# Kernel tuning notes

Hardware: AMD Instinct MI355X
Metric: run time of the kernel (lower is better)

Reference implementation:

```python
import jax, jax.numpy as jnp
import numpy as np

D_MODEL = 1024
NHEAD = 16
D_K = D_MODEL // NHEAD


def setup_inputs() -> dict:
    key = jax.random.key(0)
    ks = jax.random.split(key, 12)
    B, L = 4, 2048
    s = 1.0 / np.sqrt(D_MODEL)
    inp = {
        "query": jax.random.normal(ks[0], (B, L, D_MODEL), jnp.float32),
        "key": jax.random.normal(ks[1], (B, L, D_MODEL), jnp.float32),
        "value": jax.random.normal(ks[2], (B, L, D_MODEL), jnp.float32),
        "Wq": jax.random.normal(ks[3], (D_MODEL, D_MODEL), jnp.float32) * s,
        "bq": jnp.zeros((D_MODEL,), jnp.float32),
        "Wk": jax.random.normal(ks[4], (D_MODEL, D_MODEL), jnp.float32) * s,
        "bk": jnp.zeros((D_MODEL,), jnp.float32),
        "Wv": jax.random.normal(ks[5], (D_MODEL, D_MODEL), jnp.float32) * s,
        "bv": jnp.zeros((D_MODEL,), jnp.float32),
        "Wo": jax.random.normal(ks[6], (D_MODEL, D_MODEL), jnp.float32) * s,
        "bo": jnp.zeros((D_MODEL,), jnp.float32),
    }
    return inp


def reference(query, key, value, Wq, bq, Wk, bk, Wv, bv, Wo, bo):
    B, Lq, _ = query.shape
    Lk = key.shape[1]
    # Linear projections, split into heads: [B, H, L, d_k]
    Q = (query @ Wq + bq).reshape(B, Lq, NHEAD, D_K).transpose(0, 2, 1, 3)
    K = (key @ Wk + bk).reshape(B, Lk, NHEAD, D_K).transpose(0, 2, 1, 3)
    V = (value @ Wv + bv).reshape(B, Lk, NHEAD, D_K).transpose(0, 2, 1, 3)
    scale = 1.0 / jnp.sqrt(jnp.asarray(D_K, Q.dtype))
    scores = jnp.einsum("bhqd,bhkd->bhqk", Q, K) * scale  # [B,H,Lq,Lk]
    attn = jax.nn.softmax(scores, axis=-1)
    context = jnp.einsum("bhqk,bhkd->bhqd", attn, V)
    context = context.transpose(0, 2, 1, 3).reshape(B, Lq, D_MODEL)
    return context @ Wo + bo
```

## Files before the change

kernel.cpp:

```cpp
#include <hip/hip_runtime.h>
#include <hip/hip_bf16.h>
#include <cstdint>
#include <cstddef>


typedef unsigned short u16;
typedef __bf16 bf8v __attribute__((ext_vector_type(8)));
typedef __bf16 bf4v __attribute__((ext_vector_type(4)));
typedef float f32x4 __attribute__((ext_vector_type(4)));

#define D_MODEL 1024
#define NHEAD   16
#define DK      64
#define BATCH   4
#define SEQ     2048
#define ROWS    (BATCH * SEQ)

__device__ __forceinline__ u16 f2b(float f) {
  union { float f; unsigned int i; } x; x.f = f;
  unsigned int r = x.i + 0x7fffu + ((x.i >> 16) & 1u);
  return (u16)(r >> 16);
}
__device__ __forceinline__ ushort4 pack4(float a, float b, float c, float d) {
  union { bf4v v; ushort4 u; } x;
  x.v[0] = (__bf16)a; x.v[1] = (__bf16)b; x.v[2] = (__bf16)c; x.v[3] = (__bf16)d;
  return x.u;
}
__device__ __forceinline__ bf8v cvt8(float4 a, float4 b) {
  bf8v r;
  r[0] = (__bf16)a.x; r[1] = (__bf16)a.y; r[2] = (__bf16)a.z; r[3] = (__bf16)a.w;
  r[4] = (__bf16)b.x; r[5] = (__bf16)b.y; r[6] = (__bf16)b.z; r[7] = (__bf16)b.w;
  return r;
}
__device__ __forceinline__ void async16(const void* g, void* l) {
  __builtin_amdgcn_global_load_lds((const __attribute__((address_space(1))) void*)g,
                                   (__attribute__((address_space(3))) void*)l, 16, 0, 0);
}
#define MFMA16(a, b, c) __builtin_amdgcn_mfma_f32_16x16x32_bf16(a, b, c, 0, 0, 0)

__global__ void wtrans_cvt_kernel(const float* __restrict__ w0, const float* __restrict__ w1,
                                  const float* __restrict__ w2, const float* __restrict__ w3,
                                  u16* __restrict__ dst4) {
  __shared__ float t[32][33];
  const float* src = (blockIdx.z == 0) ? w0 : (blockIdx.z == 1) ? w1
                   : (blockIdx.z == 2) ? w2 : w3;
  u16* dst = dst4 + (size_t)blockIdx.z * D_MODEL * D_MODEL;
  const int c0 = blockIdx.x * 32, r0 = blockIdx.y * 32;
  for (int i = threadIdx.y; i < 32; i += 8)
    t[i][threadIdx.x] = src[(size_t)(r0 + i) * D_MODEL + c0 + threadIdx.x];
  __syncthreads();
  for (int i = threadIdx.y; i < 32; i += 8)
    dst[(size_t)(c0 + i) * D_MODEL + r0 + threadIdx.x] = f2b(t[threadIdx.x][i]);
}

#define BM 128
#define BN 128
#define BK 32

__global__ __launch_bounds__(256, 2) void gemm_qkv(
    const float* __restrict__ Aq, const float* __restrict__ Ak,
    const float* __restrict__ Av, const u16* __restrict__ wt,
    const float* __restrict__ bq, const float* __restrict__ bk,
    const float* __restrict__ bv, u16* __restrict__ Qw, u16* __restrict__ Kw,
    u16* __restrict__ Vt, float qscale) {
  __shared__ __align__(16) u16 As[2][BM * BK];
  __shared__ __align__(16) u16 Bs[2][BN * BK];
  const int z = blockIdx.y;
  const float* A = (z == 0) ? Aq : (z == 1) ? Ak : Av;
  const u16* Bt = wt + (size_t)z * D_MODEL * D_MODEL;
  const float* bias = (z == 0) ? bq : (z == 1) ? bk : bv;
  u16* out = (z == 0) ? Qw : (z == 1) ? Kw : Vt;
  const float oscale = (z == 0) ? qscale : 1.0f;

  const int lid = blockIdx.x;
  const int xcd = lid & 7, jj = lid >> 3;
  const int m0 = ((xcd << 3) + (jj >> 3)) * BM;
  const int n0 = (jj & 7) * BN;

  const int tid = threadIdx.x;
  const int lane = tid & 63, wave = tid >> 6;
  const int wm = wave >> 1, wn = wave & 1;
  const int quad = lane >> 4, l16 = lane & 15;
  const int K = 1024;

  f32x4 acc[4][4];
#pragma unroll
  for (int i = 0; i < 4; i++)
#pragma unroll
    for (int j = 0; j < 4; j++) acc[i][j] = (f32x4){0.f, 0.f, 0.f, 0.f};

  const int srow = tid >> 2;
  const int sch = ((tid & 3) ^ ((tid >> 3) & 3)) * 8;
  const int fsw = (quad ^ ((l16 >> 1) & 3)) * 8;
  const float* Ag0 = A + (size_t)(m0 + srow) * K + sch;
  const float* Ag1 = Ag0 + (size_t)64 * K;
  const u16* Bg = Bt + (size_t)(n0 + srow) * K + sch;

  float4 a0 = *(const float4*)(Ag0);
  float4 a1 = *(const float4*)(Ag0 + 4);
  float4 a2 = *(const float4*)(Ag1);
  float4 a3 = *(const float4*)(Ag1 + 4);
  async16(Bg, &Bs[0][tid * 8]);
  async16(Bg + (size_t)64 * K, &Bs[0][2048 + tid * 8]);
  *(bf8v*)&As[0][tid * 8]        = cvt8(a0, a1);
  *(bf8v*)&As[0][2048 + tid * 8] = cvt8(a2, a3);
  a0 = *(const float4*)(Ag0 + BK);
  a1 = *(const float4*)(Ag0 + BK + 4);
  a2 = *(const float4*)(Ag1 + BK);
  a3 = *(const float4*)(Ag1 + BK + 4);
  __syncthreads();

  int p = 0;
  for (int k0 = 0; k0 < K; k0 += BK) {
    const int kn = k0 + BK;
    if (kn < K) {
      async16(Bg + kn, &Bs[p ^ 1][tid * 8]);
      async16(Bg + (size_t)64 * K + kn, &Bs[p ^ 1][2048 + tid * 8]);
      *(bf8v*)&As[p ^ 1][tid * 8]        = cvt8(a0, a1);
      *(bf8v*)&As[p ^ 1][2048 + tid * 8] = cvt8(a2, a3);
      if (kn + BK < K) {
        a0 = *(const float4*)(Ag0 + kn + BK);
        a1 = *(const float4*)(Ag0 + kn + BK + 4);
        a2 = *(const float4*)(Ag1 + kn + BK);
        a3 = *(const float4*)(Ag1 + kn + BK + 4);
      }
    }

    bf8v af[4], bfr[4];
#pragma unroll
    for (int i = 0; i < 4; i++)
      af[i] = *(const bf8v*)&As[p][(wm * 64 + i * 16 + l16) * BK + fsw];
#pragma unroll
    for (int j = 0; j < 4; j++)
      bfr[j] = *(const bf8v*)&Bs[p][(wn * 64 + j * 16 + l16) * BK + fsw];
    if (z < 2) {
#pragma unroll
      for (int i = 0; i < 4; i++)
#pragma unroll
        for (int j = 0; j < 4; j++)
          acc[i][j] = MFMA16(bfr[j], af[i], acc[i][j]);
    } else {
#pragma unroll
      for (int i = 0; i < 4; i++)
#pragma unroll
        for (int j = 0; j < 4; j++)
          acc[i][j] = MFMA16(af[i], bfr[j], acc[i][j]);
    }
    __syncthreads();
    p ^= 1;
  }

  if (z < 2) {
#pragma unroll
    for (int i = 0; i < 4; i++) {
      const int m = m0 + wm * 64 + i * 16 + l16;
      const int b = m >> 11, l = m & 2047;
#pragma unroll
      for (int j = 0; j < 4; j++) {
        const int n = n0 + wn * 64 + j * 16 + quad * 4;
        const float4 bv4 = *(const float4*)&bias[n];
        const int h = n >> 6, d = n & 63;
        *(ushort4*)&out[(((size_t)(b * NHEAD + h) * SEQ + l) << 6) + d] =
            pack4((acc[i][j][0] + bv4.x) * oscale, (acc[i][j][1] + bv4.y) * oscale,
                  (acc[i][j][2] + bv4.z) * oscale, (acc[i][j][3] + bv4.w) * oscale);
      }
    }
  } else {
#pragma unroll
    for (int j = 0; j < 4; j++) {
      const int n = n0 + wn * 64 + j * 16 + l16;
      const float bvs = bias[n];
      const int h = n >> 6, d = n & 63;
#pragma unroll
      for (int i = 0; i < 4; i++) {
        const int row = m0 + wm * 64 + i * 16 + quad * 4;
        const int b = row >> 11, l = row & 2047;
        const int pl = (l & ~31) | ((l & 12) << 1) | ((l & 16) >> 2);
        *(ushort4*)&out[(((size_t)(b * NHEAD + h) * DK + d) << 11) + pl] =
            pack4(acc[i][j][0] + bvs, acc[i][j][1] + bvs,
                  acc[i][j][2] + bvs, acc[i][j][3] + bvs);
      }
    }
  }
}

__global__ __launch_bounds__(256, 2) void gemm_out(const u16* __restrict__ A,
                                                   const u16* __restrict__ Bt,
                                                   const float* __restrict__ bias,
                                                   float* __restrict__ out) {
  __shared__ __align__(16) u16 As[2][BM * BK];
  __shared__ __align__(16) u16 Bs[2][BN * BK];
  const int lid = blockIdx.x;
  const int xcd = lid & 7, jj = lid >> 3;
  const int m0 = ((xcd << 3) + (jj >> 3)) * BM;
  const int n0 = (jj & 7) * BN;
  const int tid = threadIdx.x;
  const int lane = tid & 63, wave = tid >> 6;
  const int wm = wave >> 1, wn = wave & 1;
  const int quad = lane >> 4, l16 = lane & 15;
  const int K = 1024;

  f32x4 acc[4][4];
#pragma unroll
  for (int i = 0; i < 4; i++)
#pragma unroll
    for (int j = 0; j < 4; j++) acc[i][j] = (f32x4){0.f, 0.f, 0.f, 0.f};

  const int srow = tid >> 2;
  const int sch = ((tid & 3) ^ ((tid >> 3) & 3)) * 8;
  const int fsw = (quad ^ ((l16 >> 1) & 3)) * 8;
  const u16* Ag = A + (size_t)(m0 + srow) * K + sch;
  const u16* Bg = Bt + (size_t)(n0 + srow) * K + sch;

  async16(Ag, &As[0][tid * 8]);
  async16(Ag + (size_t)64 * K, &As[0][2048 + tid * 8]);
  async16(Bg, &Bs[0][tid * 8]);
  async16(Bg + (size_t)64 * K, &Bs[0][2048 + tid * 8]);
  __syncthreads();

  int p = 0;
  for (int k0 = 0; k0 < K; k0 += BK) {
    const int kn = k0 + BK;
    if (kn < K) {
      async16(Ag + kn, &As[p ^ 1][tid * 8]);
      async16(Ag + (size_t)64 * K + kn, &As[p ^ 1][2048 + tid * 8]);
      async16(Bg + kn, &Bs[p ^ 1][tid * 8]);
      async16(Bg + (size_t)64 * K + kn, &Bs[p ^ 1][2048 + tid * 8]);
    }

    bf8v af[4], bfr[4];
#pragma unroll
    for (int i = 0; i < 4; i++)
      af[i] = *(const bf8v*)&As[p][(wm * 64 + i * 16 + l16) * BK + fsw];
#pragma unroll
    for (int j = 0; j < 4; j++)
      bfr[j] = *(const bf8v*)&Bs[p][(wn * 64 + j * 16 + l16) * BK + fsw];
#pragma unroll
    for (int i = 0; i < 4; i++)
#pragma unroll
      for (int j = 0; j < 4; j++)
        acc[i][j] = MFMA16(bfr[j], af[i], acc[i][j]);
    __syncthreads();
    p ^= 1;
  }

#pragma unroll
  for (int i = 0; i < 4; i++) {
    const int m = m0 + wm * 64 + i * 16 + l16;
#pragma unroll
    for (int j = 0; j < 4; j++) {
      const int n = n0 + wn * 64 + j * 16 + quad * 4;
      const float4 bv4 = *(const float4*)&bias[n];
      float4 vv;
      vv.x = acc[i][j][0] + bv4.x; vv.y = acc[i][j][1] + bv4.y;
      vv.z = acc[i][j][2] + bv4.z; vv.w = acc[i][j][3] + bv4.w;
      *(float4*)&out[(size_t)m * D_MODEL + n] = vv;
    }
  }
}

__global__ __launch_bounds__(256, 4) void attn_kernel(const u16* __restrict__ Q,
                                                      const u16* __restrict__ K,
                                                      const u16* __restrict__ Vt,
                                                      u16* __restrict__ ctx) {
  const int bh = blockIdx.x;
  const int qb = blockIdx.y * 128;
  const int tid = threadIdx.x;
  const int lane = tid & 63, wave = tid >> 6;
  const int quad = lane >> 4, l16 = lane & 15;
  const u16* Qh = Q + (size_t)bh * SEQ * DK;
  const u16* Kh = K + (size_t)bh * SEQ * DK;
  const u16* Vh = Vt + (size_t)bh * DK * SEQ;

  __shared__ __align__(16) u16 Ks[2][2][64 * 32];
  __shared__ __align__(16) u16 Vs[2][64 * 64];

  const int srow = tid >> 2;
  const int sch  = ((tid & 3) ^ ((tid >> 3) & 3)) * 8;
  const int ldst = tid * 8;
  const int fsw  = (quad ^ ((l16 >> 1) & 3)) * 8;
  const int vd   = tid >> 3;
  const int vcol = ((tid & 7) ^ ((tid >> 3) & 7)) * 8;

  bf8v qf[2][2];
#pragma unroll
  for (int qg = 0; qg < 2; qg++)
#pragma unroll
    for (int h = 0; h < 2; h++)
      qf[qg][h] = *(const bf8v*)&Qh[(size_t)(qb + wave * 32 + qg * 16 + l16) * DK + h * 32 + quad * 8];

  bf8v ones;
#pragma unroll
  for (int j = 0; j < 8; j++) ones[j] = (__bf16)1.0f;

  f32x4 o[2][4];
  f32x4 la[2];
  float m_q[2];
#pragma unroll
  for (int qg = 0; qg < 2; qg++) {
    m_q[qg] = -1e30f; la[qg] = (f32x4){0.f, 0.f, 0.f, 0.f};
#pragma unroll
    for (int d = 0; d < 4; d++) o[qg][d] = (f32x4){0.f, 0.f, 0.f, 0.f};
  }

  async16(Kh + (size_t)srow * DK + sch,      &Ks[0][0][ldst]);
  async16(Kh + (size_t)srow * DK + 32 + sch, &Ks[0][1][ldst]);
  async16(Vh + (size_t)vd * SEQ + vcol,        &Vs[0][ldst]);
  async16(Vh + (size_t)(vd + 32) * SEQ + vcol, &Vs[0][2048 + ldst]);
  __syncthreads();

  int p = 0;
  for (int kt = 0; kt < SEQ; kt += 64) {
    const int nt = kt + 64;
    if (nt < SEQ) {
      async16(Kh + (size_t)(nt + srow) * DK + sch,      &Ks[p ^ 1][0][ldst]);
      async16(Kh + (size_t)(nt + srow) * DK + 32 + sch, &Ks[p ^ 1][1][ldst]);
      async16(Vh + (size_t)vd * SEQ + nt + vcol,        &Vs[p ^ 1][ldst]);
      async16(Vh + (size_t)(vd + 32) * SEQ + nt + vcol, &Vs[p ^ 1][2048 + ldst]);
    }

    bf8v kf[4][2];
#pragma unroll
    for (int nb = 0; nb < 4; nb++)
#pragma unroll
      for (int h = 0; h < 2; h++)
        kf[nb][h] = *(const bf8v*)&Ks[p][h][(nb * 16 + l16) * 32 + fsw];

    bf8v pf[2][2];
#pragma unroll
    for (int qg = 0; qg < 2; qg++) {
      f32x4 s[4];
      __builtin_amdgcn_s_setprio(1);
#pragma unroll
      for (int nb = 0; nb < 4; nb++) {
        f32x4 t = (f32x4){0.f, 0.f, 0.f, 0.f};
        t = MFMA16(kf[nb][0], qf[qg][0], t);
        t = MFMA16(kf[nb][1], qf[qg][1], t);
        s[nb] = t;
      }
      __builtin_amdgcn_s_setprio(0);
      float t0 = fmaxf(fmaxf(s[0][0], s[0][1]), fmaxf(s[0][2], s[0][3]));
      float t1 = fmaxf(fmaxf(s[1][0], s[1][1]), fmaxf(s[1][2], s[1][3]));
      float t2 = fmaxf(fmaxf(s[2][0], s[2][1]), fmaxf(s[2][2], s[2][3]));
      float t3 = fmaxf(fmaxf(s[3][0], s[3][1]), fmaxf(s[3][2], s[3][3]));
      float mx = fmaxf(fmaxf(t0, t1), fmaxf(t2, t3));
      mx = fmaxf(mx, __shfl_xor(mx, 16));
      mx = fmaxf(mx, __shfl_xor(mx, 32));
      const float mprev = m_q[qg];
      float Mn = mprev;
      const int resc = !__all(mx - mprev <= 8.0f);
      if (resc) {
        Mn = fmaxf(mprev, mx);
        const float al = __builtin_amdgcn_exp2f(mprev - Mn);
        m_q[qg] = Mn;
        la[qg] *= al;
#pragma unroll
        for (int d = 0; d < 4; d++) o[qg][d] *= al;
      }
#pragma unroll
      for (int nb = 0; nb < 4; nb++)
#pragma unroll
        for (int r = 0; r < 4; r++)
          s[nb][r] = __builtin_amdgcn_exp2f(s[nb][r] - Mn);
#pragma unroll
      for (int kc = 0; kc < 2; kc++) {
        bf8v pw;
#pragma unroll
        for (int j = 0; j < 4; j++) {
          pw[j]     = (__bf16)s[2 * kc][j];
          pw[j + 4] = (__bf16)s[2 * kc + 1][j];
        }
        pf[qg][kc] = pw;
      }
      la[qg] = MFMA16(ones, pf[qg][0], la[qg]);
      la[qg] = MFMA16(ones, pf[qg][1], la[qg]);
    }

    bf8v vf[4][2];
#pragma unroll
    for (int dc = 0; dc < 4; dc++) {
      const int rb = (dc * 16 + l16) * 64;
#pragma unroll
      for (int kc = 0; kc < 2; kc++)
        vf[dc][kc] = *(const bf8v*)&Vs[p][rb + (((kc * 4 + quad) ^ (l16 & 7)) * 8)];
    }
    __builtin_amdgcn_s_setprio(1);
#pragma unroll
    for (int qg = 0; qg < 2; qg++)
#pragma unroll
      for (int dc = 0; dc < 4; dc++) {
        o[qg][dc] = MFMA16(vf[dc][0], pf[qg][0], o[qg][dc]);
        o[qg][dc] = MFMA16(vf[dc][1], pf[qg][1], o[qg][dc]);
      }
    __builtin_amdgcn_s_setprio(0);

    __syncthreads();
    p ^= 1;
  }

  const int b = bh >> 4, hh = bh & 15;
#pragma unroll
  for (int qg = 0; qg < 2; qg++) {
    const float inv = __builtin_amdgcn_rcpf(la[qg][0]);
    const int q = qb + wave * 32 + qg * 16 + l16;
#pragma unroll
    for (int dc = 0; dc < 4; dc++) {
      const int col = hh * 64 + dc * 16 + quad * 4;
      *(ushort4*)&ctx[(size_t)(b * SEQ + q) * D_MODEL + col] =
          pack4(o[qg][dc][0] * inv, o[qg][dc][1] * inv,
                o[qg][dc][2] * inv, o[qg][dc][3] * inv);
    }
  }
}

extern "C" void kernel_launch(void* const* d_in, const int* in_sizes, int n_in,
                              void* d_out, int out_size, void* d_ws, size_t ws_size,
                              hipStream_t stream) {
  const float* q  = (const float*)d_in[0];
  const float* k  = (const float*)d_in[1];
  const float* v  = (const float*)d_in[2];
  const float* Wq = (const float*)d_in[3];
  const float* bq = (const float*)d_in[4];
  const float* Wk = (const float*)d_in[5];
  const float* bk = (const float*)d_in[6];
  const float* Wv = (const float*)d_in[7];
  const float* bv = (const float*)d_in[8];
  const float* Wo = (const float*)d_in[9];
  const float* bo = (const float*)d_in[10];

  u16* ws  = (u16*)d_ws;
  u16* wt  = ws;
  u16* Qw  = wt + (size_t)4 * D_MODEL * D_MODEL;
  u16* Kw  = Qw + (size_t)ROWS * D_MODEL;
  u16* Vt  = Kw + (size_t)ROWS * D_MODEL;
  u16* ctx = Vt + (size_t)ROWS * D_MODEL;

  const float QSCALE = 0.18033688011112042f;

  wtrans_cvt_kernel<<<dim3(32, 32, 4), dim3(32, 8), 0, stream>>>(Wq, Wk, Wv, Wo, wt);

  gemm_qkv<<<dim3(512, 3), 256, 0, stream>>>(q, k, v, wt, bq, bk, bv, Qw, Kw, Vt, QSCALE);

  attn_kernel<<<dim3(BATCH * NHEAD, SEQ / 128), 256, 0, stream>>>(Qw, Kw, Vt, ctx);

  gemm_out<<<512, 256, 0, stream>>>(ctx, wt + (size_t)3 * D_MODEL * D_MODEL, bo,
                                    (float*)d_out);
}
```

Baseline: 384.0 us.

## Double GEMM K-tile depth to 64 with wider swizzle and MFMA priority

Raises BK from 32 to 64 in the QKV and output-projection GEMMs, which halves the number of K iterations and barriers. The load mapping and the XOR swizzle are reworked for 64-wide rows (8 chunks per row, 4 row groups per thread). The change also brackets the MFMA block with s_setprio so that compute waves get priority. Shared memory doubles to 64KB per block, which may limit occupancy at the 2-block launch bound, and register pressure grows from the extra prefetch registers.

```diff
diff --git a/kernel.cpp b/kernel.cpp
--- a/kernel.cpp
+++ b/kernel.cpp
@@ -55,7 +55,8 @@
 
 #define BM 128
 #define BN 128
-#define BK 32
+#define BK 64
+#define NT (1024 / BK)
 
 __global__ __launch_bounds__(256, 2) void gemm_qkv(
     const float* __restrict__ Aq, const float* __restrict__ Ak,
@@ -89,63 +90,82 @@
 #pragma unroll
     for (int j = 0; j < 4; j++) acc[i][j] = (f32x4){0.f, 0.f, 0.f, 0.f};
 
-  const int srow = tid >> 2;
-  const int sch = ((tid & 3) ^ ((tid >> 3) & 3)) * 8;
-  const int fsw = (quad ^ ((l16 >> 1) & 3)) * 8;
-  const float* Ag0 = A + (size_t)(m0 + srow) * K + sch;
-  const float* Ag1 = Ag0 + (size_t)64 * K;
-  const u16* Bg = Bt + (size_t)(n0 + srow) * K + sch;
-
-  float4 a0 = *(const float4*)(Ag0);
-  float4 a1 = *(const float4*)(Ag0 + 4);
-  float4 a2 = *(const float4*)(Ag1);
-  float4 a3 = *(const float4*)(Ag1 + 4);
-  async16(Bg, &Bs[0][tid * 8]);
-  async16(Bg + (size_t)64 * K, &Bs[0][2048 + tid * 8]);
-  *(bf8v*)&As[0][tid * 8]        = cvt8(a0, a1);
-  *(bf8v*)&As[0][2048 + tid * 8] = cvt8(a2, a3);
-  a0 = *(const float4*)(Ag0 + BK);
-  a1 = *(const float4*)(Ag0 + BK + 4);
-  a2 = *(const float4*)(Ag1 + BK);
-  a3 = *(const float4*)(Ag1 + BK + 4);
+  const int s8 = tid >> 3;
+  const int lc = ((tid & 7) ^ ((tid >> 4) & 7)) * 8;
+  const int fk = (l16 >> 1) & 7;
+  const float* Agt = A + (size_t)(m0 + s8) * K + lc;
+  const u16* Bgt = Bt + (size_t)(n0 + s8) * K + lc;
+
+  float4 ar[8];
+#pragma unroll
+  for (int m = 0; m < 4; m++) {
+    ar[2 * m]     = *(const float4*)(Agt + (size_t)m * 32 * K);
+    ar[2 * m + 1] = *(const float4*)(Agt + (size_t)m * 32 * K + 4);
+  }
+#pragma unroll
+  for (int m = 0; m < 4; m++)
+    async16(Bgt + (size_t)m * 32 * K, &Bs[0][m * 2048 + tid * 8]);
+#pragma unroll
+  for (int m = 0; m < 4; m++)
+    *(bf8v*)&As[0][m * 2048 + tid * 8] = cvt8(ar[2 * m], ar[2 * m + 1]);
+#pragma unroll
+  for (int m = 0; m < 4; m++) {
+    ar[2 * m]     = *(const float4*)(Agt + (size_t)m * 32 * K + BK);
+    ar[2 * m + 1] = *(const float4*)(Agt + (size_t)m * 32 * K + BK + 4);
+  }
   __syncthreads();
 
   int p = 0;
-  for (int k0 = 0; k0 < K; k0 += BK) {
-    const int kn = k0 + BK;
+  for (int t = 0; t < NT; t++) {
+    const int kn = (t + 1) * BK;
     if (kn < K) {
-      async16(Bg + kn, &Bs[p ^ 1][tid * 8]);
-      async16(Bg + (size_t)64 * K + kn, &Bs[p ^ 1][2048 + tid * 8]);
-      *(bf8v*)&As[p ^ 1][tid * 8]        = cvt8(a0, a1);
-      *(bf8v*)&As[p ^ 1][2048 + tid * 8] = cvt8(a2, a3);
+#pragma unroll
+      for (int m = 0; m < 4; m++)
+        async16(Bgt + (size_t)m * 32 * K + kn, &Bs[p ^ 1][m * 2048 + tid * 8]);
+#pragma unroll
+      for (int m = 0; m < 4; m++)
+        *(bf8v*)&As[p ^ 1][m * 2048 + tid * 8] = cvt8(ar[2 * m], ar[2 * m + 1]);
       if (kn + BK < K) {
-        a0 = *(const float4*)(Ag0 + kn + BK);
-        a1 = *(const float4*)(Ag0 + kn + BK + 4);
-        a2 = *(const float4*)(Ag1 + kn + BK);
-        a3 = *(const float4*)(Ag1 + kn + BK + 4);
-      }
-    }
-
-    bf8v af[4], bfr[4];
+#pragma unroll
+        for (int m = 0; m < 4; m++) {
+          ar[2 * m]     = *(const float4*)(Agt + (size_t)m * 32 * K + kn + BK);
+          ar[2 * m + 1] = *(const float4*)(Agt + (size_t)m * 32 * K + kn + BK + 4);
+        }
+      }
+    }
+
+    bf8v af[4][2], bfr[4][2];
 #pragma unroll
     for (int i = 0; i < 4; i++)
-      af[i] = *(const bf8v*)&As[p][(wm * 64 + i * 16 + l16) * BK + fsw];
+#pragma unroll
+      for (int h = 0; h < 2; h++)
+        af[i][h] = *(const bf8v*)&As[p][(wm * 64 + i * 16 + l16) * BK +
+                                        (((h * 4 + quad) ^ fk) * 8)];
 #pragma unroll
     for (int j = 0; j < 4; j++)
-      bfr[j] = *(const bf8v*)&Bs[p][(wn * 64 + j * 16 + l16) * BK + fsw];
+#pragma unroll
+      for (int h = 0; h < 2; h++)
+        bfr[j][h] = *(const bf8v*)&Bs[p][(wn * 64 + j * 16 + l16) * BK +
+                                         (((h * 4 + quad) ^ fk) * 8)];
+    __builtin_amdgcn_s_setprio(1);
     if (z < 2) {
 #pragma unroll
       for (int i = 0; i < 4; i++)
 #pragma unroll
-        for (int j = 0; j < 4; j++)
-          acc[i][j] = MFMA16(bfr[j], af[i], acc[i][j]);
+        for (int j = 0; j < 4; j++) {
+          acc[i][j] = MFMA16(bfr[j][0], af[i][0], acc[i][j]);
+          acc[i][j] = MFMA16(bfr[j][1], af[i][1], acc[i][j]);
+        }
     } else {
 #pragma unroll
       for (int i = 0; i < 4; i++)
 #pragma unroll
-        for (int j = 0; j < 4; j++)
-          acc[i][j] = MFMA16(af[i], bfr[j], acc[i][j]);
-    }
+        for (int j = 0; j < 4; j++) {
+          acc[i][j] = MFMA16(af[i][0], bfr[j][0], acc[i][j]);
+          acc[i][j] = MFMA16(af[i][1], bfr[j][1], acc[i][j]);
+        }
+    }
+    __builtin_amdgcn_s_setprio(0);
     __syncthreads();
     p ^= 1;
   }
@@ -206,40 +226,52 @@
 #pragma unroll
     for (int j = 0; j < 4; j++) acc[i][j] = (f32x4){0.f, 0.f, 0.f, 0.f};
 
-  const int srow = tid >> 2;
-  const int sch = ((tid & 3) ^ ((tid >> 3) & 3)) * 8;
-  const int fsw = (quad ^ ((l16 >> 1) & 3)) * 8;
-  const u16* Ag = A + (size_t)(m0 + srow) * K + sch;
-  const u16* Bg = Bt + (size_t)(n0 + srow) * K + sch;
-
-  async16(Ag, &As[0][tid * 8]);
-  async16(Ag + (size_t)64 * K, &As[0][2048 + tid * 8]);
-  async16(Bg, &Bs[0][tid * 8]);
-  async16(Bg + (size_t)64 * K, &Bs[0][2048 + tid * 8]);
+  const int s8 = tid >> 3;
+  const int lc = ((tid & 7) ^ ((tid >> 4) & 7)) * 8;
+  const int fk = (l16 >> 1) & 7;
+  const u16* Agt = A + (size_t)(m0 + s8) * K + lc;
+  const u16* Bgt = Bt + (size_t)(n0 + s8) * K + lc;
+
+#pragma unroll
+  for (int m = 0; m < 4; m++) {
+    async16(Agt + (size_t)m * 32 * K, &As[0][m * 2048 + tid * 8]);
+    async16(Bgt + (size_t)m * 32 * K, &Bs[0][m * 2048 + tid * 8]);
+  }
   __syncthreads();
 
   int p = 0;
-  for (int k0 = 0; k0 < K; k0 += BK) {
-    const int kn = k0 + BK;
+  for (int t = 0; t < NT; t++) {
+    const int kn = (t + 1) * BK;
     if (kn < K) {
-      async16(Ag + kn, &As[p ^ 1][tid * 8]);
-      async16(Ag + (size_t)64 * K + kn, &As[p ^ 1][2048 + tid * 8]);
-      async16(Bg + kn, &Bs[p ^ 1][tid * 8]);
-      async16(Bg + (size_t)64 * K + kn, &Bs[p ^ 1][2048 + tid * 8]);
-    }
-
-    bf8v af[4], bfr[4];
+#pragma unroll
+      for (int m = 0; m < 4; m++) {
+        async16(Agt + (size_t)m * 32 * K + kn, &As[p ^ 1][m * 2048 + tid * 8]);
+        async16(Bgt + (size_t)m * 32 * K + kn, &Bs[p ^ 1][m * 2048 + tid * 8]);
+      }
+    }
+
+    bf8v af[4][2], bfr[4][2];
 #pragma unroll
     for (int i = 0; i < 4; i++)
-      af[i] = *(const bf8v*)&As[p][(wm * 64 + i * 16 + l16) * BK + fsw];
+#pragma unroll
+      for (int h = 0; h < 2; h++)
+        af[i][h] = *(const bf8v*)&As[p][(wm * 64 + i * 16 + l16) * BK +
+                                        (((h * 4 + quad) ^ fk) * 8)];
 #pragma unroll
     for (int j = 0; j < 4; j++)
-      bfr[j] = *(const bf8v*)&Bs[p][(wn * 64 + j * 16 + l16) * BK + fsw];
+#pragma unroll
+      for (int h = 0; h < 2; h++)
+        bfr[j][h] = *(const bf8v*)&Bs[p][(wn * 64 + j * 16 + l16) * BK +
+                                         (((h * 4 + quad) ^ fk) * 8)];
+    __builtin_amdgcn_s_setprio(1);
 #pragma unroll
     for (int i = 0; i < 4; i++)
 #pragma unroll
-      for (int j = 0; j < 4; j++)
-        acc[i][j] = MFMA16(bfr[j], af[i], acc[i][j]);
+      for (int j = 0; j < 4; j++) {
+        acc[i][j] = MFMA16(bfr[j][0], af[i][0], acc[i][j]);
+        acc[i][j] = MFMA16(bfr[j][1], af[i][1], acc[i][j]);
+      }
+    __builtin_amdgcn_s_setprio(0);
     __syncthreads();
     p ^= 1;
   }
```

Result: faster. 352.9 us (-8.1%).
